# Kernel optimization log

Hardware: AMD Instinct MI355X
Metric: run time of the kernel (lower is better)

Reference implementation:

```python
import jax, jax.numpy as jnp
import numpy as np

CROP = 48
THRESHOLD = 0.5
IOU_THRESHOLD = 0.5


def _conv(x, w, b):
    # x: [N,H,W,C], w: [kh,kw,Cin,Cout]
    y = jax.lax.conv_general_dilated(x, w, (1, 1), 'VALID',
                                     dimension_numbers=('NHWC', 'HWIO', 'NHWC'))
    return y + b


def _prelu(x, a):
    # a broadcasts over the channel-last axis
    return jnp.where(x >= 0, x, a * x)


def _maxpool(x, k, s, p):
    return jax.lax.reduce_window(x, -jnp.inf, jax.lax.max,
                                 (1, k, k, 1), (1, s, s, 1),
                                 ((0, 0), (p, p), (p, p), (0, 0)))


def _nms_keep(boxes, scores, valid, iou_thr):
    # fixed-shape greedy NMS (torchvision semantics: suppress iou > thr)
    N = boxes.shape[0]
    s = jnp.where(valid, scores, -jnp.inf)
    order = jnp.argsort(-s)
    b = boxes[order]
    x1, y1, x2, y2 = b[:, 0], b[:, 1], b[:, 2], b[:, 3]
    area = (x2 - x1) * (y2 - y1)
    xx1 = jnp.maximum(x1[:, None], x1[None, :])
    yy1 = jnp.maximum(y1[:, None], y1[None, :])
    xx2 = jnp.minimum(x2[:, None], x2[None, :])
    yy2 = jnp.minimum(y2[:, None], y2[None, :])
    inter = jnp.clip(xx2 - xx1, 0.0) * jnp.clip(yy2 - yy1, 0.0)
    iou = inter / (area[:, None] + area[None, :] - inter + 1e-12)
    keep0 = valid[order]
    idx = jnp.arange(N)

    def body(i, keep):
        sup = (iou[i] > iou_thr) & (idx > i) & keep[i] & keep
        return keep & ~sup

    keep_sorted = jax.lax.fori_loop(0, N, body, keep0)
    return jnp.zeros(N, bool).at[order].set(keep_sorted)


def setup_inputs() -> dict:
    key = jax.random.key(0)
    ks = jax.random.split(key, 24)
    H = W = 1024
    N = 2048
    image = jax.random.uniform(ks[0], (H, W, 3), jnp.float32) * 255.0
    x1 = jax.random.uniform(ks[1], (N,), jnp.float32) * (W - 130)
    y1 = jax.random.uniform(ks[2], (N,), jnp.float32) * (H - 130)
    bw = 20.0 + jax.random.uniform(ks[3], (N,), jnp.float32) * 100.0
    bh = 20.0 + jax.random.uniform(ks[4], (N,), jnp.float32) * 100.0
    bboxes = jnp.stack([x1, y1, x1 + bw, y1 + bh], axis=1)
    rn = lambda k, sh, s: jax.random.normal(k, sh, jnp.float32) * s
    return {
        'bboxes': bboxes, 'image': image,
        'conv1_w': rn(ks[5], (3, 3, 3, 32), 0.05), 'conv1_b': rn(ks[6], (32,), 0.01),
        'prelu1': 0.25 * jnp.ones((32,), jnp.float32),
        'conv2_w': rn(ks[7], (3, 3, 32, 64), 0.05), 'conv2_b': rn(ks[8], (64,), 0.01),
        'prelu2': 0.25 * jnp.ones((64,), jnp.float32),
        'conv3_w': rn(ks[9], (3, 3, 64, 64), 0.05), 'conv3_b': rn(ks[10], (64,), 0.01),
        'prelu3': 0.25 * jnp.ones((64,), jnp.float32),
        'conv4_w': rn(ks[11], (2, 2, 64, 128), 0.05), 'conv4_b': rn(ks[12], (128,), 0.01),
        'prelu4': 0.25 * jnp.ones((128,), jnp.float32),
        'fc5_w': rn(ks[13], (256, 1152), 0.02), 'fc5_b': rn(ks[14], (256,), 0.01),
        'prelu5': 0.25 * jnp.ones((256,), jnp.float32),
        'fc6a_w': rn(ks[15], (2, 256), 0.1), 'fc6a_b': rn(ks[16], (2,), 0.01),
        'fc6b_w': rn(ks[17], (4, 256), 0.1), 'fc6b_b': rn(ks[18], (4,), 0.01),
    }


def reference(bboxes, image, conv1_w, conv1_b, prelu1, conv2_w, conv2_b, prelu2,
              conv3_w, conv3_b, prelu3, conv4_w, conv4_b, prelu4,
              fc5_w, fc5_b, prelu5, fc6a_w, fc6a_b, fc6b_w, fc6b_b):
    H, W = image.shape[0], image.shape[1]
    N = bboxes.shape[0]
    # preprocess (torch: (x - 127.5) * 0.0078125)
    data = (image - 127.5) * 0.0078125  # [H,W,3]
    # clip boxes in place like the torch forward
    bx1 = jnp.clip(bboxes[:, 0], 0.0, None)
    by1 = jnp.clip(bboxes[:, 1], 0.0, None)
    bx2 = jnp.clip(bboxes[:, 2], None, float(W))
    by2 = jnp.clip(bboxes[:, 3], None, float(H))
    bb = jnp.stack([bx1, by1, bx2, by2], axis=1)  # clipped boxes [N,4]
    # integer crop windows (torch .int() truncation; coords >= 0)
    ib = bb.astype(jnp.int32)
    cw = jnp.maximum(ib[:, 2] - ib[:, 0], 1)
    ch = jnp.maximum(ib[:, 3] - ib[:, 1], 1)
    # nearest-neighbor resize to 48x48 (F.interpolate default mode='nearest')
    r = jnp.arange(CROP, dtype=jnp.int32)
    xs = ib[:, 0:1] + (r[None, :] * cw[:, None]) // CROP  # [N,48]
    ys = ib[:, 1:2] + (r[None, :] * ch[:, None]) // CROP  # [N,48]
    crops = data[ys[:, :, None], xs[:, None, :], :]  # [N,48,48,3] gather
    # CNN trunk
    h = _maxpool(_prelu(_conv(crops, conv1_w, conv1_b), prelu1), 3, 2, 1)
    h = _maxpool(_prelu(_conv(h, conv2_w, conv2_b), prelu2), 3, 2, 0)
    h = _maxpool(_prelu(_conv(h, conv3_w, conv3_b), prelu3), 2, 2, 0)
    h = _prelu(_conv(h, conv4_w, conv4_b), prelu4)  # [N,3,3,128]
    h = jnp.transpose(h, (0, 3, 1, 2)).reshape(N, -1)  # NCHW flatten like torch -> [N,1152]
    h = _prelu(h @ fc5_w.T + fc5_b, prelu5)  # [N,256]
    cls = jax.nn.softmax(h @ fc6a_w.T + fc6a_b, axis=1)  # [N,2]
    reg = h @ fc6b_w.T + fc6b_b  # [N,4]
    score = cls[:, 1]
    valid = score >= THRESHOLD
    w = bb[:, 2] - bb[:, 0]
    hgt = bb[:, 3] - bb[:, 1]
    out = jnp.stack([bb[:, 0] + reg[:, 0] * w,
                     bb[:, 1] + reg[:, 1] * hgt,
                     bb[:, 2] + reg[:, 2] * w,
                     bb[:, 3] + reg[:, 3] * hgt], axis=1)  # [N,4]
    keep = _nms_keep(out, score, valid, IOU_THRESHOLD)
    return jnp.where(keep[:, None], out, 0.0)
```

## Files before the change

### kernel.cpp

```cpp
#include <hip/hip_runtime.h>
#include <math.h>
#include <stdint.h>

#define NBOX 2048

#define P1_RS 25
#define P1_CS 576
#define P1_SZ 18432

__device__ __forceinline__ void fma4(float4& a, float s, const float4& w) {
  a.x = fmaf(s, w.x, a.x); a.y = fmaf(s, w.y, a.y);
  a.z = fmaf(s, w.z, a.z); a.w = fmaf(s, w.w, a.w);
}
__device__ __forceinline__ float4 max4(float4 a, float4 b) {
  return make_float4(fmaxf(a.x,b.x), fmaxf(a.y,b.y), fmaxf(a.z,b.z), fmaxf(a.w,b.w));
}
__device__ __forceinline__ float4 max34(float4 a, float4 b, float4 c) {
  return max4(max4(a, b), c);
}
__device__ __forceinline__ float4 prelu4(float4 v, float4 a) {
  float4 r;
  r.x = v.x >= 0.f ? v.x : a.x*v.x;
  r.y = v.y >= 0.f ? v.y : a.y*v.y;
  r.z = v.z >= 0.f ? v.z : a.z*v.z;
  r.w = v.w >= 0.f ? v.w : a.w*v.w;
  return r;
}
__device__ __forceinline__ float4 shfl4(float4 v, int src) {
  float4 r;
  r.x = __shfl(v.x, src, 64); r.y = __shfl(v.y, src, 64);
  r.z = __shfl(v.z, src, 64); r.w = __shfl(v.w, src, 64);
  return r;
}

__global__ __launch_bounds__(256) void k1_crop_conv1(
    const float* __restrict__ bboxes, const float* __restrict__ image,
    const float* __restrict__ w1, const float* __restrict__ b1, const float* __restrict__ a1,
    float* __restrict__ p1ws, int box0)
{
  __shared__ float crop[48*48*3];
  __shared__ float w1s[27*32];
  __shared__ float b1s[32], a1s[32];
  const int tid = threadIdx.x;
  const int n = box0 + blockIdx.x;

  for (int idx = tid; idx < 27*32; idx += 256) w1s[idx] = w1[idx];
  if (tid < 32) { b1s[tid] = b1[tid]; a1s[tid] = a1[tid]; }

  float f0 = bboxes[n*4+0], f1 = bboxes[n*4+1], f2 = bboxes[n*4+2], f3 = bboxes[n*4+3];
  float bx1 = fmaxf(f0, 0.f), by1 = fmaxf(f1, 0.f);
  float bx2 = fminf(f2, 1024.f), by2 = fminf(f3, 1024.f);
  int ix1 = (int)bx1, iy1 = (int)by1, ix2 = (int)bx2, iy2 = (int)by2;
  int cw = ix2 - ix1; if (cw < 1) cw = 1;
  int ch = iy2 - iy1; if (ch < 1) ch = 1;

  for (int idx = tid; idx < 6912; idx += 256) {
    int c = idx % 3; int t = idx / 3; int j = t % 48; int i = t / 48;
    int gx = ix1 + (j * cw) / 48;
    int gy = iy1 + (i * ch) / 48;
    float v = image[(gy*1024 + gx)*3 + c];
    crop[idx] = (v - 127.5f) * 0.0078125f;
  }
  __syncthreads();

  float* p1o = p1ws + (size_t)blockIdx.x * P1_SZ;

  for (int slot = tid; slot < 1104; slot += 256) {
    int cq = slot & 7;
    int t2 = slot >> 3;
    int pjq = t2 % 6;
    int pi  = t2 / 6;
    int pj0 = pjq * 4;
    int c0 = 2*pj0 - 1;
    float4 bias  = *(const float4*)&b1s[cq*4];
    float4 alpha = *(const float4*)&a1s[cq*4];
    float4 mx[4];
#pragma unroll
    for (int t = 0; t < 4; t++) mx[t] = make_float4(-3.0e38f,-3.0e38f,-3.0e38f,-3.0e38f);

#pragma unroll
    for (int dr = 0; dr < 3; dr++) {
      int r = 2*pi - 1 + dr;
      if (r < 0 || r > 45) continue;
      float4 acc[9];
#pragma unroll
      for (int c = 0; c < 9; c++) acc[c] = bias;
#pragma unroll
      for (int kh = 0; kh < 3; kh++) {
        int row = r + kh;
        float s[33];
#pragma unroll
        for (int d = 0; d < 11; d++) {
          int cc = c0 + d; cc = cc < 0 ? 0 : (cc > 47 ? 47 : cc);
          int base = row*144 + cc*3;
          s[d*3+0] = crop[base+0];
          s[d*3+1] = crop[base+1];
          s[d*3+2] = crop[base+2];
        }
#pragma unroll
        for (int kw = 0; kw < 3; kw++) {
#pragma unroll
          for (int ci = 0; ci < 3; ci++) {
            float4 w = *(const float4*)&w1s[((kh*3+kw)*3+ci)*32 + cq*4];
#pragma unroll
            for (int c = 0; c < 9; c++) fma4(acc[c], s[(c+kw)*3+ci], w);
          }
        }
      }
#pragma unroll
      for (int c = 0; c < 9; c++) {
        int cabs = c0 + c;
        if (cabs < 0 || cabs > 45) continue;
        float4 pv = prelu4(acc[c], alpha);
#pragma unroll
        for (int t = 0; t < 4; t++) {
          if (c >= 2*t && c <= 2*t+2) mx[t] = max4(mx[t], pv);
        }
      }
    }
#pragma unroll
    for (int t = 0; t < 4; t++) {
      int pj = pj0 + t;
      if (pj < 23) {
        int base = pi*P1_RS + pj;
        p1o[(cq*4+0)*P1_CS + base] = mx[t].x;
        p1o[(cq*4+1)*P1_CS + base] = mx[t].y;
        p1o[(cq*4+2)*P1_CS + base] = mx[t].z;
        p1o[(cq*4+3)*P1_CS + base] = mx[t].w;
      }
    }
  }
}

#define K2_LOADW(W, CI, KH) { \
  const float* wp_ = w2 + (((KH)*3)*32 + (CI))*64 + co0; \
  W[0] = *(const float4*)(wp_);            W[1] = *(const float4*)(wp_ + 4); \
  W[2] = *(const float4*)(wp_ + 2048);     W[3] = *(const float4*)(wp_ + 2052); \
  W[4] = *(const float4*)(wp_ + 4096);     W[5] = *(const float4*)(wp_ + 4100); }

#define K2_COMP(W, CI, KH) { \
  const float* ip_ = &in_s[(CI)*P1_CS + (rl+(KH))*P1_RS + j0]; \
  float s_[9]; \
  _Pragma("unroll") for (int d_ = 0; d_ < 9; d_++) s_[d_] = ip_[d_]; \
  _Pragma("unroll") for (int kw_ = 0; kw_ < 3; kw_++) { \
    _Pragma("unroll") for (int jj_ = 0; jj_ < 7; jj_++) { \
      fma4(acc[jj_][0], s_[jj_+kw_], W[kw_*2]); \
      fma4(acc[jj_][1], s_[jj_+kw_], W[kw_*2+1]); } } }

#define K2_STORE8(PJ, LO, HI) { \
  float* d_ = p2o + (size_t)co0*120 + pi*12 + (PJ); \
  float4 lo_ = (LO), hi_ = (HI); \
  d_[0]   = lo_.x; d_[120] = lo_.y; d_[240] = lo_.z; d_[360] = lo_.w; \
  d_[480] = hi_.x; d_[600] = hi_.y; d_[720] = hi_.z; d_[840] = hi_.w; }

__global__ __launch_bounds__(512, 4) void k2_conv2(
    const float* __restrict__ w2, const float* __restrict__ b2, const float* __restrict__ a2,
    const float* __restrict__ p1ws, float* __restrict__ p2ws)
{
  __shared__ float in_s[P1_SZ];
  const int tid = threadIdx.x;
  const float* p1o = p1ws + (size_t)blockIdx.x * P1_SZ;
  float* p2o = p2ws + (size_t)blockIdx.x * 7680;

  for (int i4 = tid; i4 < P1_SZ/4; i4 += 512)
    *(float4*)&in_s[i4*4] = *(const float4*)&p1o[i4*4];
  __syncthreads();

  const int wav = __builtin_amdgcn_readfirstlane(tid >> 6);
  const int lane = tid & 63;
  int jt = lane / 21;
  int rl = lane - jt * 21;
  if (lane == 63) { jt = 2; rl = 20; }
  const int j0 = jt * 7;
  const int co0 = wav * 8;

  float4 bL = *(const float4*)&b2[co0];
  float4 bH = *(const float4*)&b2[co0+4];
  float4 aL = *(const float4*)&a2[co0];
  float4 aH = *(const float4*)&a2[co0+4];

  float4 acc[7][2];
#pragma unroll
  for (int jj = 0; jj < 7; jj++) { acc[jj][0] = bL; acc[jj][1] = bH; }

  float4 wA[6], wB[6];
  K2_LOADW(wA, 0, 0);
#pragma unroll 1
  for (int ci = 0; ci < 32; ci += 2) {
    K2_LOADW(wB, ci, 1);
    K2_COMP(wA, ci, 0);
    K2_LOADW(wA, ci, 2);
    K2_COMP(wB, ci, 1);
    K2_LOADW(wB, ci+1, 0);
    K2_COMP(wA, ci, 2);
    K2_LOADW(wA, ci+1, 1);
    K2_COMP(wB, ci+1, 0);
    K2_LOADW(wB, ci+1, 2);
    K2_COMP(wA, ci+1, 1);
    if (ci + 2 < 32) K2_LOADW(wA, ci+2, 0);
    K2_COMP(wB, ci+1, 2);
  }

#pragma unroll
  for (int jj = 0; jj < 7; jj++) {
    acc[jj][0] = prelu4(acc[jj][0], aL);
    acc[jj][1] = prelu4(acc[jj][1], aH);
  }

#pragma unroll
  for (int jj = 0; jj < 7; jj++) {
#pragma unroll
    for (int h = 0; h < 2; h++) {
      float4 v = acc[jj][h];
      float4 d1 = shfl4(v, lane + 1);
      float4 d2 = shfl4(v, lane + 2);
      acc[jj][h] = max34(v, d1, d2);
    }
  }
  float4 r0[2], r1[2];
#pragma unroll
  for (int h = 0; h < 2; h++) {
    r0[h] = shfl4(acc[0][h], lane + 21);
    r1[h] = shfl4(acc[1][h], lane + 21);
  }

  if (((rl & 1) == 0) && rl <= 18) {
    const int pi = rl >> 1;
    if (jt == 0) {
      K2_STORE8(0, max34(acc[0][0],acc[1][0],acc[2][0]), max34(acc[0][1],acc[1][1],acc[2][1]));
      K2_STORE8(1, max34(acc[2][0],acc[3][0],acc[4][0]), max34(acc[2][1],acc[3][1],acc[4][1]));
      K2_STORE8(2, max34(acc[4][0],acc[5][0],acc[6][0]), max34(acc[4][1],acc[5][1],acc[6][1]));
      K2_STORE8(3, max34(acc[6][0],r0[0],r1[0]),          max34(acc[6][1],r0[1],r1[1]));
    } else if (jt == 1) {
      K2_STORE8(4, max34(acc[1][0],acc[2][0],acc[3][0]), max34(acc[1][1],acc[2][1],acc[3][1]));
      K2_STORE8(5, max34(acc[3][0],acc[4][0],acc[5][0]), max34(acc[3][1],acc[4][1],acc[5][1]));
      K2_STORE8(6, max34(acc[5][0],acc[6][0],r0[0]),     max34(acc[5][1],acc[6][1],r0[1]));
    } else {
      K2_STORE8(7, max34(acc[0][0],acc[1][0],acc[2][0]), max34(acc[0][1],acc[1][1],acc[2][1]));
      K2_STORE8(8, max34(acc[2][0],acc[3][0],acc[4][0]), max34(acc[2][1],acc[3][1],acc[4][1]));
      K2_STORE8(9, max34(acc[4][0],acc[5][0],acc[6][0]), max34(acc[4][1],acc[5][1],acc[6][1]));
    }
  }
}

#define K3_LOADW(W, CI, KH) { \
  const float* wp_ = w3 + (((KH)*3)*64 + (CI))*64 + co0; \
  W[0] = *(const float4*)(wp_);            W[1] = *(const float4*)(wp_ + 4); \
  W[2] = *(const float4*)(wp_ + 4096);     W[3] = *(const float4*)(wp_ + 4100); \
  W[4] = *(const float4*)(wp_ + 8192);     W[5] = *(const float4*)(wp_ + 8196); }

#define K3_COMP(W, CI, KH) { \
  const float* ip_ = ibase + (CI)*120 + (KH)*12; \
  float2 sA_ = *(const float2*)(ip_); \
  float2 sB_ = *(const float2*)(ip_ + 2); \
  float s_[4] = {sA_.x, sA_.y, sB_.x, sB_.y}; \
  _Pragma("unroll") for (int kw_ = 0; kw_ < 3; kw_++) { \
    _Pragma("unroll") for (int c_ = 0; c_ < 2; c_++) { \
      fma4(acc[c_][0], s_[c_+kw_], W[kw_*2]); \
      fma4(acc[c_][1], s_[c_+kw_], W[kw_*2+1]); } } }

__global__ __launch_bounds__(512, 4) void k3_conv3(
    const float* __restrict__ w3, const float* __restrict__ b3, const float* __restrict__ a3,
    const float* __restrict__ p2ws, float* __restrict__ p3ws)
{
  __shared__ float in_s[15376];
  const int tid = threadIdx.x;
  const float* p2o = p2ws + (size_t)(blockIdx.x*2) * 7680;
  float* p3o0 = p3ws + (size_t)(blockIdx.x*2) * 1024;

  for (int i4 = tid; i4 < 3840; i4 += 512) {
    int bb = (i4 >= 1920) ? 1 : 0;
    int k = i4 - bb*1920;
    *(float4*)&in_s[bb*7688 + k*4] = *(const float4*)&p2o[(size_t)bb*7680 + k*4];
  }
  __syncthreads();

  const int wav = __builtin_amdgcn_readfirstlane(tid >> 6);
  const int lane = tid & 63;
  const int b  = lane >> 5;
  const int r  = (lane >> 2) & 7;
  const int cg = lane & 3;
  const int co0 = wav * 8;

  float4 bL = *(const float4*)&b3[co0];
  float4 bH = *(const float4*)&b3[co0+4];
  float4 aL = *(const float4*)&a3[co0];
  float4 aH = *(const float4*)&a3[co0+4];

  float4 acc[2][2];
  acc[0][0] = bL; acc[0][1] = bH; acc[1][0] = bL; acc[1][1] = bH;

  const float* ibase = &in_s[b*7688 + r*12 + cg*2];

  float4 wA[6], wB[6];
  K3_LOADW(wA, 0, 0);
#pragma unroll 1
  for (int ci = 0; ci < 64; ci += 2) {
    K3_LOADW(wB, ci, 1);
    K3_COMP(wA, ci, 0);
    K3_LOADW(wA, ci, 2);
    K3_COMP(wB, ci, 1);
    K3_LOADW(wB, ci+1, 0);
    K3_COMP(wA, ci, 2);
    K3_LOADW(wA, ci+1, 1);
    K3_COMP(wB, ci+1, 0);
    K3_LOADW(wB, ci+1, 2);
    K3_COMP(wA, ci+1, 1);
    if (ci + 2 < 64) K3_LOADW(wA, ci+2, 0);
    K3_COMP(wB, ci+1, 2);
  }

  float4 hm[2];
#pragma unroll
  for (int h = 0; h < 2; h++) {
    float4 p0 = prelu4(acc[0][h], h ? aH : aL);
    float4 p1 = prelu4(acc[1][h], h ? aH : aL);
    hm[h] = max4(p0, p1);
  }
  float4 o[2];
#pragma unroll
  for (int h = 0; h < 2; h++) {
    float4 d = shfl4(hm[h], lane + 4);
    o[h] = max4(hm[h], d);
  }
  if ((r & 1) == 0) {
    const int pi = r >> 1;
    float* d = p3o0 + b*1024 + (size_t)co0*16 + pi*4 + cg;
    d[0]   = o[0].x; d[16]  = o[0].y; d[32]  = o[0].z; d[48]  = o[0].w;
    d[64]  = o[1].x; d[80]  = o[1].y; d[96]  = o[1].z; d[112] = o[1].w;
  }
}

__global__ __launch_bounds__(128) void k4_conv4(
    const float* __restrict__ w4, const float* __restrict__ b4, const float* __restrict__ a4,
    const float* __restrict__ p3ws, float* __restrict__ c4ws)
{
  __shared__ float p3s[1024];
  __shared__ float w4s[64*128];
  __shared__ float b4s[128], a4s[128];
  const int tid = threadIdx.x;
  const float* p3o = p3ws + (size_t)blockIdx.x * 1024;
  float* c4o = c4ws + (size_t)blockIdx.x * 1152;
  b4s[tid] = b4[tid]; a4s[tid] = a4[tid];
  for (int idx4 = tid; idx4 < 256; idx4 += 128)
    *(float4*)&p3s[idx4*4] = *(const float4*)&p3o[idx4*4];

  const int slot = tid;
  const bool active = slot < 96;
  const int cq = slot & 31, rl = slot >> 5;
  float4 acc[3];
  bool first = true;
  for (int cg = 0; cg < 4; cg++) {
    __syncthreads();
    for (int idx4 = tid; idx4 < 2048; idx4 += 128) {
      int co4 = idx4 & 31, kkcl = idx4 >> 5;
      int khkw = kkcl >> 4, cl = kkcl & 15;
      *(float4*)&w4s[kkcl*128 + co4*4] =
          *(const float4*)&w4[(khkw*64 + cg*16 + cl)*128 + co4*4];
    }
    __syncthreads();
    if (active) {
      if (first) {
        float4 b = *(const float4*)&b4s[cq*4];
        acc[0]=b; acc[1]=b; acc[2]=b; first=false;
      }
      for (int cl = 0; cl < 16; cl++) {
        int ci = cg*16 + cl;
#pragma unroll
        for (int kh = 0; kh < 2; kh++) {
          float4 sv = *(const float4*)&p3s[ci*16 + (rl+kh)*4];
          float s[4] = {sv.x, sv.y, sv.z, sv.w};
#pragma unroll
          for (int kw = 0; kw < 2; kw++) {
            float4 w = *(const float4*)&w4s[((kh*2+kw)*16+cl)*128 + cq*4];
#pragma unroll
            for (int v = 0; v < 3; v++) fma4(acc[v], s[v+kw], w);
          }
        }
      }
    }
  }
  if (active) {
    float4 alpha = *(const float4*)&a4s[cq*4];
#pragma unroll
    for (int v = 0; v < 3; v++) {
      float4 p = prelu4(acc[v], alpha);
      c4o[(cq*4+0)*9 + rl*3 + v] = p.x;
      c4o[(cq*4+1)*9 + rl*3 + v] = p.y;
      c4o[(cq*4+2)*9 + rl*3 + v] = p.z;
      c4o[(cq*4+3)*9 + rl*3 + v] = p.w;
    }
  }
}

__global__ __launch_bounds__(256) void k5_fc(
    const float* __restrict__ fc5w, const float* __restrict__ fc5b, const float* __restrict__ a5,
    const float* __restrict__ w6a, const float* __restrict__ b6a,
    const float* __restrict__ w6b, const float* __restrict__ b6b,
    const float* __restrict__ bboxes, const float* __restrict__ c4ws,
    float* __restrict__ ws_scores, float* __restrict__ ws_boxes, int box0)
{
  __shared__ float c4s[8*1152];
  __shared__ float hs[8*256];
  __shared__ float l6[8][6];
  __shared__ float b5s[256], a5s[256];
  const int tid = threadIdx.x;
  const int lb0 = blockIdx.x * 8;
  b5s[tid] = fc5b[tid]; a5s[tid] = a5[tid];
  for (int idx4 = tid; idx4 < 2304; idx4 += 256)
    *(float4*)&c4s[idx4*4] = *(const float4*)&c4ws[(size_t)lb0*1152 + idx4*4];
  __syncthreads();

  const int og = tid & 31, bl = tid >> 5;
  float acc[8] = {0,0,0,0,0,0,0,0};
  const float* cbase = &c4s[bl*1152];
  for (int k = 0; k < 1152; k += 4) {
    float4 a = *(const float4*)&cbase[k];
#pragma unroll
    for (int u = 0; u < 8; u++) {
      int o = og + 32*u;
      float4 w = *(const float4*)&fc5w[(size_t)o*1152 + k];
      acc[u] += a.x*w.x + a.y*w.y + a.z*w.z + a.w*w.w;
    }
  }
#pragma unroll
  for (int u = 0; u < 8; u++) {
    int o = og + 32*u;
    float h = acc[u] + b5s[o];
    h = h >= 0.f ? h : a5s[o]*h;
    hs[bl*256 + o] = h;
  }
  __syncthreads();
  if (tid < 48) {
    int b = tid / 6, oi = tid % 6;
    const float* w = (oi < 2) ? &w6a[oi*256] : &w6b[(oi-2)*256];
    float d = (oi < 2) ? b6a[oi] : b6b[oi-2];
    const float* hh = &hs[b*256];
    for (int k = 0; k < 256; k++) d += hh[k]*w[k];
    l6[b][oi] = d;
  }
  __syncthreads();
  if (tid < 8) {
    int n = box0 + lb0 + tid;
    float l0 = l6[tid][0], l1 = l6[tid][1];
    float m = fmaxf(l0, l1);
    float e0 = expf(l0-m), e1 = expf(l1-m);
    float score = e1/(e0+e1);
    float r0 = l6[tid][2], r1 = l6[tid][3], r2 = l6[tid][4], r3 = l6[tid][5];
    float f0 = bboxes[n*4+0], f1 = bboxes[n*4+1], f2 = bboxes[n*4+2], f3 = bboxes[n*4+3];
    float bx1 = fmaxf(f0, 0.f), by1 = fmaxf(f1, 0.f);
    float bx2 = fminf(f2, 1024.f), by2 = fminf(f3, 1024.f);
    float w_ = bx2-bx1, h_ = by2-by1;
    ws_scores[n] = score;
    float4 ob = make_float4(bx1 + r0*w_, by1 + r1*h_, bx2 + r2*w_, by2 + r3*h_);
    *(float4*)&ws_boxes[n*4] = ob;
  }
}

__global__ __launch_bounds__(1024) void k6a_sort(
    const float* __restrict__ ws_scores, const float* __restrict__ ws_boxes,
    int* __restrict__ sidx_ws, float* __restrict__ sbox_ws,
    float* __restrict__ area_ws, int* __restrict__ nv_ws)
{
  __shared__ float skey[2048];
  __shared__ int   sidx[2048];
  const int tid = threadIdx.x;
  for (int i = tid; i < 2048; i += 1024) {
    float s = ws_scores[i];
    skey[i] = (s >= 0.5f) ? s : -INFINITY;
    sidx[i] = i;
  }
  __syncthreads();
  for (int k = 2; k <= 2048; k <<= 1) {
    for (int j = k >> 1; j > 0; j >>= 1) {
      for (int i = tid; i < 2048; i += 1024) {
        int ixj = i ^ j;
        if (ixj > i) {
          float a = skey[i], b = skey[ixj];
          int ia = sidx[i], ib = sidx[ixj];
          bool up = ((i & k) == 0);
          bool aAfterB = (a < b) || (a == b && ia > ib);
          if (up ? aAfterB : !aAfterB) {
            skey[i] = b; skey[ixj] = a; sidx[i] = ib; sidx[ixj] = ia;
          }
        }
      }
      __syncthreads();
    }
  }
  if (tid == 0) nv_ws[0] = 2048;
  __syncthreads();
  for (int i = tid; i < 2048; i += 1024) {
    if (skey[i] == -INFINITY && (i == 0 || skey[i-1] != -INFINITY)) nv_ws[0] = i;
    int n = sidx[i];
    sidx_ws[i] = n;
    float4 b = *(const float4*)&ws_boxes[n*4];
    *(float4*)&sbox_ws[i*4] = b;
    area_ws[i] = (b.z-b.x)*(b.w-b.y);
  }
}

__global__ __launch_bounds__(256) void k6b_iou(
    const int* __restrict__ nv_ws, const float* __restrict__ sbox_ws,
    const float* __restrict__ area_ws, unsigned long long* __restrict__ M)
{
  const int nv = nv_ws[0];
  int gt = blockIdx.x*256 + threadIdx.x;
  for (int w = gt; w < 2048*32; w += 128*256) {
    int i = w >> 5, wg = w & 31;
    if (i >= nv) continue;
    float4 bi = *(const float4*)&sbox_ws[i*4];
    float ai = area_ws[i];
    unsigned long long m = 0;
    int jbase = wg*64;
    if (jbase + 63 > i) {
      for (int jj = 0; jj < 64; jj++) {
        int j = jbase + jj;
        if (j <= i) continue;
        float4 bj = *(const float4*)&sbox_ws[j*4];
        float xx1 = fmaxf(bi.x, bj.x), yy1 = fmaxf(bi.y, bj.y);
        float xx2 = fminf(bi.z, bj.z), yy2 = fminf(bi.w, bj.w);
        float iw = fmaxf(xx2-xx1, 0.f), ih = fmaxf(yy2-yy1, 0.f);
        float inter = iw*ih;
        float iou = inter / (ai + area_ws[j] - inter + 1e-12f);
        if (iou > 0.5f) m |= (1ull << jj);
      }
    }
    M[w] = m;
  }
}

__global__ __launch_bounds__(1024) void k6c_scan(
    const int* __restrict__ nv_ws, const int* __restrict__ sidx_ws,
    const float* __restrict__ sbox_ws, const unsigned long long* __restrict__ M,
    float* __restrict__ out)
{
  __shared__ unsigned long long Msh[128*32];
  __shared__ unsigned long long rem_sh[32];
  const int tid = threadIdx.x;
  const int nv = nv_ws[0];
  unsigned long long rem = 0;

  for (int c0 = 0; c0 < 2048; c0 += 128) {
    if (c0 >= nv) break;
    for (int w = tid; w < 128*32; w += 1024) {
      int i = c0 + (w >> 5);
      if (i < nv) Msh[w] = M[(size_t)i*32 + (w & 31)];
    }
    __syncthreads();
    if (tid < 64) {
      int iend = c0 + 128; if (iend > nv) iend = nv;
      for (int i = c0; i < iend; i += 4) {
        unsigned long long m0=0, m1=0, m2=0, m3=0;
        int base = (i - c0) << 5;
        if (tid < 32) {
          m0 = Msh[base + tid];
          if (i+1 < iend) m1 = Msh[base + 32 + tid];
          if (i+2 < iend) m2 = Msh[base + 64 + tid];
          if (i+3 < iend) m3 = Msh[base + 96 + tid];
        }
        unsigned long long rw = __shfl(rem, (i >> 6), 64);
        if (!((rw >> (i & 63)) & 1ull)) rem |= m0;
        if (i+1 < iend) {
          rw = __shfl(rem, ((i+1) >> 6), 64);
          if (!((rw >> ((i+1) & 63)) & 1ull)) rem |= m1;
        }
        if (i+2 < iend) {
          rw = __shfl(rem, ((i+2) >> 6), 64);
          if (!((rw >> ((i+2) & 63)) & 1ull)) rem |= m2;
        }
        if (i+3 < iend) {
          rw = __shfl(rem, ((i+3) >> 6), 64);
          if (!((rw >> ((i+3) & 63)) & 1ull)) rem |= m3;
        }
      }
    }
    __syncthreads();
  }
  if (tid < 32) rem_sh[tid] = rem;
  __syncthreads();
  for (int i = tid; i < 2048; i += 1024) {
    bool keep = (i < nv) && !((rem_sh[i >> 6] >> (i & 63)) & 1ull);
    int n = sidx_ws[i];
    float4 b = *(const float4*)&sbox_ws[i*4];
    float4 o = keep ? b : make_float4(0.f,0.f,0.f,0.f);
    *(float4*)&out[n*4] = o;
  }
}

extern "C" void kernel_launch(void* const* d_in, const int* in_sizes, int n_in,
                              void* d_out, int out_size, void* d_ws, size_t ws_size,
                              hipStream_t stream)
{
  const float* bboxes = (const float*)d_in[0];
  const float* image  = (const float*)d_in[1];
  const float* w1 = (const float*)d_in[2];  const float* b1 = (const float*)d_in[3];  const float* a1 = (const float*)d_in[4];
  const float* w2 = (const float*)d_in[5];  const float* b2 = (const float*)d_in[6];  const float* a2 = (const float*)d_in[7];
  const float* w3 = (const float*)d_in[8];  const float* b3 = (const float*)d_in[9];  const float* a3 = (const float*)d_in[10];
  const float* w4 = (const float*)d_in[11]; const float* b4 = (const float*)d_in[12]; const float* a4 = (const float*)d_in[13];
  const float* fc5w = (const float*)d_in[14]; const float* fc5b = (const float*)d_in[15]; const float* a5 = (const float*)d_in[16];
  const float* w6a = (const float*)d_in[17]; const float* b6a = (const float*)d_in[18];
  const float* w6b = (const float*)d_in[19]; const float* b6b = (const float*)d_in[20];
  float* out = (float*)d_out;

  char* ws = (char*)d_ws;
  size_t off = 0;
  auto alloc = [&](size_t bytes) -> size_t {
    size_t p = off; off += (bytes + 255) & ~(size_t)255; return p;
  };
  size_t o_scores = alloc(NBOX*4);
  size_t o_boxes  = alloc(NBOX*16);
  size_t o_sidx   = alloc(NBOX*4);
  size_t o_sbox   = alloc(NBOX*16);
  size_t o_area   = alloc(NBOX*4);
  size_t o_nv     = alloc(256);
  size_t o_M      = alloc((size_t)NBOX*32*8);
  size_t fixed = off;
  const size_t perbox = (size_t)(P1_SZ + 7680 + 1024 + 1152) * 4;

  int B = NBOX;
  if (fixed + (size_t)B*perbox > ws_size) {
    size_t avail = ws_size > fixed ? ws_size - fixed : 0;
    B = (int)(avail / perbox);
    B &= ~7;
    if (B < 8) B = 8;
    if (B > NBOX) B = NBOX;
  }
  size_t o_p1 = alloc((size_t)B*P1_SZ*4);
  size_t o_p2 = alloc((size_t)B*7680*4);
  size_t o_p3 = alloc((size_t)B*1024*4);
  size_t o_c4 = alloc((size_t)B*1152*4);

  float* ws_scores = (float*)(ws + o_scores);
  float* ws_boxes  = (float*)(ws + o_boxes);
  int*   sidxp     = (int*)(ws + o_sidx);
  float* sboxp     = (float*)(ws + o_sbox);
  float* areap     = (float*)(ws + o_area);
  int*   nvp       = (int*)(ws + o_nv);
  unsigned long long* Mp = (unsigned long long*)(ws + o_M);
  float* p1p = (float*)(ws + o_p1);
  float* p2p = (float*)(ws + o_p2);
  float* p3p = (float*)(ws + o_p3);
  float* c4p = (float*)(ws + o_c4);

  for (int c0 = 0; c0 < NBOX; c0 += B) {
    int Bc = NBOX - c0; if (Bc > B) Bc = B;
    k1_crop_conv1<<<Bc, 256, 0, stream>>>(bboxes, image, w1, b1, a1, p1p, c0);
    k2_conv2<<<Bc, 512, 0, stream>>>(w2, b2, a2, p1p, p2p);
    k3_conv3<<<Bc/2, 512, 0, stream>>>(w3, b3, a3, p2p, p3p);
    k4_conv4<<<Bc, 128, 0, stream>>>(w4, b4, a4, p3p, c4p);
    k5_fc<<<Bc/8, 256, 0, stream>>>(fc5w, fc5b, a5, w6a, b6a, w6b, b6b,
                                    bboxes, c4p, ws_scores, ws_boxes, c0);
  }
  k6a_sort<<<1, 1024, 0, stream>>>(ws_scores, ws_boxes, sidxp, sboxp, areap, nvp);
  k6b_iou<<<128, 256, 0, stream>>>(nvp, sboxp, areap, Mp);
  k6c_scan<<<1, 1024, 0, stream>>>(nvp, sidxp, sboxp, Mp, out);
}
```

Measured before the change: 1.694 ms.

## Halve conv2/conv3 shared input via channel halves; restructure conv4 to register-blocked waves

conv2 and conv3 now load their input into shared memory in two channel halves instead of all at once. This halves LDS use per block, and launch bounds are raised so more blocks can fit per CU, at the cost of an extra barrier round per block. conv4 is rewritten so each 512-thread block handles four boxes with register-prefetched weights read directly from global memory, replacing the 128-thread per-box version that staged weights in shared memory. Threads for spatial positions beyond nine still compute redundant results, so some lanes do wasted work.

Result: slower. 3.810 ms (+125.0%).

```diff
diff --git a/kernel.cpp b/kernel.cpp
--- a/kernel.cpp
+++ b/kernel.cpp
@@ -138,8 +138,8 @@
   W[2] = *(const float4*)(wp_ + 2048);     W[3] = *(const float4*)(wp_ + 2052); \
   W[4] = *(const float4*)(wp_ + 4096);     W[5] = *(const float4*)(wp_ + 4100); }
 
-#define K2_COMP(W, CI, KH) { \
-  const float* ip_ = &in_s[(CI)*P1_CS + (rl+(KH))*P1_RS + j0]; \
+#define K2_COMP(W, CIL, KH) { \
+  const float* ip_ = &in_s[(CIL)*P1_CS + (rl+(KH))*P1_RS + j0]; \
   float s_[9]; \
   _Pragma("unroll") for (int d_ = 0; d_ < 9; d_++) s_[d_] = ip_[d_]; \
   _Pragma("unroll") for (int kw_ = 0; kw_ < 3; kw_++) { \
@@ -153,18 +153,14 @@
   d_[0]   = lo_.x; d_[120] = lo_.y; d_[240] = lo_.z; d_[360] = lo_.w; \
   d_[480] = hi_.x; d_[600] = hi_.y; d_[720] = hi_.z; d_[840] = hi_.w; }
 
-__global__ __launch_bounds__(512, 4) void k2_conv2(
+__global__ __launch_bounds__(512, 8) void k2_conv2(
     const float* __restrict__ w2, const float* __restrict__ b2, const float* __restrict__ a2,
     const float* __restrict__ p1ws, float* __restrict__ p2ws)
 {
-  __shared__ float in_s[P1_SZ];
+  __shared__ float in_s[9216];
   const int tid = threadIdx.x;
   const float* p1o = p1ws + (size_t)blockIdx.x * P1_SZ;
   float* p2o = p2ws + (size_t)blockIdx.x * 7680;
-
-  for (int i4 = tid; i4 < P1_SZ/4; i4 += 512)
-    *(float4*)&in_s[i4*4] = *(const float4*)&p1o[i4*4];
-  __syncthreads();
 
   const int wav = __builtin_amdgcn_readfirstlane(tid >> 6);
   const int lane = tid & 63;
@@ -183,22 +179,31 @@
 #pragma unroll
   for (int jj = 0; jj < 7; jj++) { acc[jj][0] = bL; acc[jj][1] = bH; }
 
-  float4 wA[6], wB[6];
-  K2_LOADW(wA, 0, 0);
 #pragma unroll 1
-  for (int ci = 0; ci < 32; ci += 2) {
-    K2_LOADW(wB, ci, 1);
-    K2_COMP(wA, ci, 0);
-    K2_LOADW(wA, ci, 2);
-    K2_COMP(wB, ci, 1);
-    K2_LOADW(wB, ci+1, 0);
-    K2_COMP(wA, ci, 2);
-    K2_LOADW(wA, ci+1, 1);
-    K2_COMP(wB, ci+1, 0);
-    K2_LOADW(wB, ci+1, 2);
-    K2_COMP(wA, ci+1, 1);
-    if (ci + 2 < 32) K2_LOADW(wA, ci+2, 0);
-    K2_COMP(wB, ci+1, 2);
+  for (int h = 0; h < 2; h++) {
+    __syncthreads();
+    for (int i4 = tid; i4 < 2304; i4 += 512)
+      *(float4*)&in_s[i4*4] = *(const float4*)&p1o[h*9216 + i4*4];
+    __syncthreads();
+
+    const int cb = h*16;
+    float4 wA[6], wB[6];
+    K2_LOADW(wA, cb+0, 0);
+#pragma unroll 1
+    for (int ci = 0; ci < 16; ci += 2) {
+      K2_LOADW(wB, cb+ci, 1);
+      K2_COMP(wA, ci, 0);
+      K2_LOADW(wA, cb+ci, 2);
+      K2_COMP(wB, ci, 1);
+      K2_LOADW(wB, cb+ci+1, 0);
+      K2_COMP(wA, ci, 2);
+      K2_LOADW(wA, cb+ci+1, 1);
+      K2_COMP(wB, ci+1, 0);
+      K2_LOADW(wB, cb+ci+1, 2);
+      K2_COMP(wA, ci+1, 1);
+      if (ci + 2 < 16) K2_LOADW(wA, cb+ci+2, 0);
+      K2_COMP(wB, ci+1, 2);
+    }
   }
 
 #pragma unroll
@@ -249,8 +254,8 @@
   W[2] = *(const float4*)(wp_ + 4096);     W[3] = *(const float4*)(wp_ + 4100); \
   W[4] = *(const float4*)(wp_ + 8192);     W[5] = *(const float4*)(wp_ + 8196); }
 
-#define K3_COMP(W, CI, KH) { \
-  const float* ip_ = ibase + (CI)*120 + (KH)*12; \
+#define K3_COMP(W, CIL, KH) { \
+  const float* ip_ = ibase + (CIL)*120 + (KH)*12; \
   float2 sA_ = *(const float2*)(ip_); \
   float2 sB_ = *(const float2*)(ip_ + 2); \
   float s_[4] = {sA_.x, sA_.y, sB_.x, sB_.y}; \
@@ -259,21 +264,14 @@
       fma4(acc[c_][0], s_[c_+kw_], W[kw_*2]); \
       fma4(acc[c_][1], s_[c_+kw_], W[kw_*2+1]); } } }
 
-__global__ __launch_bounds__(512, 4) void k3_conv3(
+__global__ __launch_bounds__(512, 8) void k3_conv3(
     const float* __restrict__ w3, const float* __restrict__ b3, const float* __restrict__ a3,
     const float* __restrict__ p2ws, float* __restrict__ p3ws)
 {
-  __shared__ float in_s[15376];
+  __shared__ float in_s[7696];
   const int tid = threadIdx.x;
   const float* p2o = p2ws + (size_t)(blockIdx.x*2) * 7680;
   float* p3o0 = p3ws + (size_t)(blockIdx.x*2) * 1024;
-
-  for (int i4 = tid; i4 < 3840; i4 += 512) {
-    int bb = (i4 >= 1920) ? 1 : 0;
-    int k = i4 - bb*1920;
-    *(float4*)&in_s[bb*7688 + k*4] = *(const float4*)&p2o[(size_t)bb*7680 + k*4];
-  }
-  __syncthreads();
 
   const int wav = __builtin_amdgcn_readfirstlane(tid >> 6);
   const int lane = tid & 63;
@@ -290,24 +288,36 @@
   float4 acc[2][2];
   acc[0][0] = bL; acc[0][1] = bH; acc[1][0] = bL; acc[1][1] = bH;
 
-  const float* ibase = &in_s[b*7688 + r*12 + cg*2];
-
-  float4 wA[6], wB[6];
-  K3_LOADW(wA, 0, 0);
+  const float* ibase = &in_s[b*3848 + r*12 + cg*2];
+
 #pragma unroll 1
-  for (int ci = 0; ci < 64; ci += 2) {
-    K3_LOADW(wB, ci, 1);
-    K3_COMP(wA, ci, 0);
-    K3_LOADW(wA, ci, 2);
-    K3_COMP(wB, ci, 1);
-    K3_LOADW(wB, ci+1, 0);
-    K3_COMP(wA, ci, 2);
-    K3_LOADW(wA, ci+1, 1);
-    K3_COMP(wB, ci+1, 0);
-    K3_LOADW(wB, ci+1, 2);
-    K3_COMP(wA, ci+1, 1);
-    if (ci + 2 < 64) K3_LOADW(wA, ci+2, 0);
-    K3_COMP(wB, ci+1, 2);
+  for (int h = 0; h < 2; h++) {
+    __syncthreads();
+    for (int i4 = tid; i4 < 1920; i4 += 512) {
+      int bb = (i4 >= 960) ? 1 : 0;
+      int k = i4 - bb*960;
+      *(float4*)&in_s[bb*3848 + k*4] = *(const float4*)&p2o[(size_t)bb*7680 + h*3840 + k*4];
+    }
+    __syncthreads();
+
+    const int cb = h*32;
+    float4 wA[6], wB[6];
+    K3_LOADW(wA, cb+0, 0);
+#pragma unroll 1
+    for (int ci = 0; ci < 32; ci += 2) {
+      K3_LOADW(wB, cb+ci, 1);
+      K3_COMP(wA, ci, 0);
+      K3_LOADW(wA, cb+ci, 2);
+      K3_COMP(wB, ci, 1);
+      K3_LOADW(wB, cb+ci+1, 0);
+      K3_COMP(wA, ci, 2);
+      K3_LOADW(wA, cb+ci+1, 1);
+      K3_COMP(wB, ci+1, 0);
+      K3_LOADW(wB, cb+ci+1, 2);
+      K3_COMP(wA, ci+1, 1);
+      if (ci + 2 < 32) K3_LOADW(wA, cb+ci+2, 0);
+      K3_COMP(wB, ci+1, 2);
+    }
   }
 
   float4 hm[2];
@@ -331,64 +341,70 @@
   }
 }
 
-__global__ __launch_bounds__(128) void k4_conv4(
+#define K4_LOADW(W, CI) { \
+  const float* wp_ = w4 + (CI)*128 + co0; \
+  W[0] = *(const float4*)(wp_);           W[1] = *(const float4*)(wp_ + 4); \
+  W[2] = *(const float4*)(wp_ + 8192);    W[3] = *(const float4*)(wp_ + 8196); \
+  W[4] = *(const float4*)(wp_ + 16384);   W[5] = *(const float4*)(wp_ + 16388); \
+  W[6] = *(const float4*)(wp_ + 24576);   W[7] = *(const float4*)(wp_ + 24580); }
+
+#define K4_COMP(W, CI) { \
+  const float* ip_ = base + (CI)*16; \
+  float i00 = ip_[0], i01 = ip_[1], i10 = ip_[4], i11 = ip_[5]; \
+  fma4(acc0, i00, W[0]); fma4(acc1, i00, W[1]); \
+  fma4(acc0, i01, W[2]); fma4(acc1, i01, W[3]); \
+  fma4(acc0, i10, W[4]); fma4(acc1, i10, W[5]); \
+  fma4(acc0, i11, W[6]); fma4(acc1, i11, W[7]); }
+
+__global__ __launch_bounds__(512) void k4_conv4(
     const float* __restrict__ w4, const float* __restrict__ b4, const float* __restrict__ a4,
     const float* __restrict__ p3ws, float* __restrict__ c4ws)
 {
-  __shared__ float p3s[1024];
-  __shared__ float w4s[64*128];
-  __shared__ float b4s[128], a4s[128];
+  __shared__ float p3s[4*1032];
   const int tid = threadIdx.x;
-  const float* p3o = p3ws + (size_t)blockIdx.x * 1024;
-  float* c4o = c4ws + (size_t)blockIdx.x * 1152;
-  b4s[tid] = b4[tid]; a4s[tid] = a4[tid];
-  for (int idx4 = tid; idx4 < 256; idx4 += 128)
-    *(float4*)&p3s[idx4*4] = *(const float4*)&p3o[idx4*4];
-
-  const int slot = tid;
-  const bool active = slot < 96;
-  const int cq = slot & 31, rl = slot >> 5;
-  float4 acc[3];
-  bool first = true;
-  for (int cg = 0; cg < 4; cg++) {
-    __syncthreads();
-    for (int idx4 = tid; idx4 < 2048; idx4 += 128) {
-      int co4 = idx4 & 31, kkcl = idx4 >> 5;
-      int khkw = kkcl >> 4, cl = kkcl & 15;
-      *(float4*)&w4s[kkcl*128 + co4*4] =
-          *(const float4*)&w4[(khkw*64 + cg*16 + cl)*128 + co4*4];
-    }
-    __syncthreads();
-    if (active) {
-      if (first) {
-        float4 b = *(const float4*)&b4s[cq*4];
-        acc[0]=b; acc[1]=b; acc[2]=b; first=false;
-      }
-      for (int cl = 0; cl < 16; cl++) {
-        int ci = cg*16 + cl;
-#pragma unroll
-        for (int kh = 0; kh < 2; kh++) {
-          float4 sv = *(const float4*)&p3s[ci*16 + (rl+kh)*4];
-          float s[4] = {sv.x, sv.y, sv.z, sv.w};
-#pragma unroll
-          for (int kw = 0; kw < 2; kw++) {
-            float4 w = *(const float4*)&w4s[((kh*2+kw)*16+cl)*128 + cq*4];
-#pragma unroll
-            for (int v = 0; v < 3; v++) fma4(acc[v], s[v+kw], w);
-          }
-        }
-      }
-    }
-  }
-  if (active) {
-    float4 alpha = *(const float4*)&a4s[cq*4];
-#pragma unroll
-    for (int v = 0; v < 3; v++) {
-      float4 p = prelu4(acc[v], alpha);
-      c4o[(cq*4+0)*9 + rl*3 + v] = p.x;
-      c4o[(cq*4+1)*9 + rl*3 + v] = p.y;
-      c4o[(cq*4+2)*9 + rl*3 + v] = p.z;
-      c4o[(cq*4+3)*9 + rl*3 + v] = p.w;
+  const int bi0 = blockIdx.x * 4;
+
+  for (int i4 = tid; i4 < 1024; i4 += 512) {
+    int bb = i4 >> 8, k = i4 & 255;
+    *(float4*)&p3s[bb*1032 + k*4] = *(const float4*)&p3ws[(size_t)(bi0+bb)*1024 + k*4];
+  }
+  __syncthreads();
+
+  const int wav = __builtin_amdgcn_readfirstlane(tid >> 6);
+  const int lane = tid & 63;
+  const int bx = lane >> 4;
+  const int sp = lane & 15;
+  const bool act = sp < 9;
+  const int sq = act ? sp : 8;
+  const int r = sq / 3, c = sq - 3*r;
+  const float* base = &p3s[bx*1032 + r*4 + c];
+  float* c4o = c4ws + (size_t)(bi0+bx)*1152;
+
+#pragma unroll 1
+  for (int p = 0; p < 2; p++) {
+    const int co0 = p*64 + wav*8;
+    float4 bL = *(const float4*)&b4[co0];
+    float4 bH = *(const float4*)&b4[co0+4];
+    float4 aL = *(const float4*)&a4[co0];
+    float4 aH = *(const float4*)&a4[co0+4];
+    float4 acc0 = bL, acc1 = bH;
+
+    float4 wA[8], wB[8];
+    K4_LOADW(wA, 0);
+#pragma unroll 1
+    for (int ci = 0; ci < 64; ci += 2) {
+      K4_LOADW(wB, ci+1);
+      K4_COMP(wA, ci);
+      if (ci + 2 < 64) K4_LOADW(wA, ci+2);
+      K4_COMP(wB, ci+1);
+    }
+
+    if (act) {
+      float4 p0 = prelu4(acc0, aL);
+      float4 p1 = prelu4(acc1, aH);
+      float* d = c4o + (size_t)co0*9 + sp;
+      d[0]  = p0.x; d[9]  = p0.y; d[18] = p0.z; d[27] = p0.w;
+      d[36] = p1.x; d[45] = p1.y; d[54] = p1.z; d[63] = p1.w;
     }
   }
 }
@@ -648,7 +664,7 @@
     k1_crop_conv1<<<Bc, 256, 0, stream>>>(bboxes, image, w1, b1, a1, p1p, c0);
     k2_conv2<<<Bc, 512, 0, stream>>>(w2, b2, a2, p1p, p2p);
     k3_conv3<<<Bc/2, 512, 0, stream>>>(w3, b3, a3, p2p, p3p);
-    k4_conv4<<<Bc, 128, 0, stream>>>(w4, b4, a4, p3p, c4p);
+    k4_conv4<<<Bc/4, 512, 0, stream>>>(w4, b4, a4, p3p, c4p);
     k5_fc<<<Bc/8, 256, 0, stream>>>(fc5w, fc5b, a5, w6a, b6a, w6b, b6b,
                                     bboxes, c4p, ws_scores, ws_boxes, c0);
   }
```
